# Kernel tuning notes

Hardware: AMD Instinct MI355X
Metric: run time of the kernel (lower is better)

Reference implementation:

```python
import jax, jax.numpy as jnp
import numpy as np

M_FEATS = 1536      # number of proposals (docstring: [M, K])
K_DIM = 128         # feature dim per docstring example
NUM_CLASSES = 16    # label vocabulary; torch.unique loop becomes a fixed class sweep


def setup_inputs() -> dict:
    key = jax.random.key(0)
    k1, k2 = jax.random.split(key)
    features = jax.random.normal(k1, (M_FEATS, K_DIM), dtype=jnp.float32)
    labels = jax.random.randint(k2, (M_FEATS,), 0, NUM_CLASSES, dtype=jnp.int32)
    # ious all ones -> keep = (ious >= 0.5) is all-True, so the boolean filter is identity
    ious = jnp.ones((M_FEATS,), dtype=jnp.float32)
    return {"features": features, "labels": labels, "ious": ious}


def reference(features, labels, ious):
    # reweight_func='none' -> coef = ones_like(ious); keep mask is all-True by construction
    coef = jnp.ones_like(ious)
    # similarity [M, M]; coef broadcasts over columns, matching `similarity * coef` in torch
    sim = jnp.matmul(features, features.T) * coef[None, :]
    m = sim.shape[0]
    eye = jnp.eye(m, dtype=sim.dtype)
    # ground set term: logdet(similarity + 0.5 I)  (mask_ground is all ones)
    ground = jnp.linalg.slogdet(sim + 0.5 * eye)[1]

    # Per-label logdet of the submatrix S_c + 0.5 I_{n_c}. Instead of extracting a
    # variable-size submatrix (not jit-able), embed it in a full [M, M] matrix that is
    # block-diagonal: class block = S_c + 0.5 I, off-class diagonal = 1. Its logdet
    # equals logdet(S_c + 0.5 I). Absent classes give identity -> logdet 0, matching
    # torch.unique skipping them.
    onehot = (labels[:, None] == jnp.arange(NUM_CLASSES, dtype=labels.dtype)[None, :])
    onehot = onehot.astype(sim.dtype)  # [M, C]

    def class_logdet(mask):  # mask: [M] 0/1 indicator for one class
        A = sim * (mask[:, None] * mask[None, :]) + jnp.diag(0.5 * mask + (1.0 - mask))
        return jnp.linalg.slogdet(A)[1]

    per_class = jax.vmap(class_logdet)(onehot.T)  # [C]
    loss = jnp.sum(per_class) - ground
    return loss  # scalar; .mean() of a scalar is itself
```

## Files before the change

kernel.cpp:

```cpp
#include <hip/hip_runtime.h>
#include <math.h>


#define M_FEATS 1536
#define K_DIM 128
#define NUM_CLASSES 16
#define GRAM_ELEMS (K_DIM * K_DIM)
#define PIDX(i) ((i) + ((i) >> 4))
#define SENT 0x13579BDF
#define MP 104
#define ALD 132

typedef short bf16x8 __attribute__((ext_vector_type(8)));
typedef float f32x4 __attribute__((ext_vector_type(4)));

__device__ __forceinline__ short f2bf(float x) {
    unsigned u = __float_as_uint(x);
    u += 0x7FFFu + ((u >> 16) & 1u);
    return (short)(u >> 16);
}

__device__ __forceinline__ float chol128(
    float A[8][8], const int t, const int rg, const int cg,
    const int i0, const int j0,
    float4* panLo, float4* panHi, float4* wshLo, float4* wshHi, float* logp)
{
    if (rg == 0) {
#pragma unroll
        for (int q = 0; q < 8; ++q) {
            panLo[PIDX(j0 + q)] = make_float4(A[0][q], A[1][q], A[2][q], A[3][q]);
            panHi[PIDX(j0 + q)] = make_float4(A[4][q], A[5][q], A[6][q], A[7][q]);
        }
    }

#pragma unroll 1
    for (int s = 0; s < 16; ++s) {
        const int k = 8 * s;
        __syncthreads();

        if (t < K_DIM) {
            float4 dL[8], dH[8];
#pragma unroll
            for (int c = 0; c < 8; ++c) {
                dL[c] = panLo[PIDX(k + c)];
                dH[c] = panHi[PIDX(k + c)];
            }
            float4 aL = panLo[PIDX(t)], aH = panHi[PIDX(t)];

            float D[8][8];
#pragma unroll
            for (int c = 0; c < 8; ++c) {
                D[0][c] = dL[c].x; D[1][c] = dL[c].y;
                D[2][c] = dL[c].z; D[3][c] = dL[c].w;
                D[4][c] = dH[c].x; D[5][c] = dH[c].y;
                D[6][c] = dH[c].z; D[7][c] = dH[c].w;
            }

            float L[8][8], ic[8];
            float prod = 1.0f;
#pragma unroll
            for (int c = 0; c < 8; ++c) {
                float v = D[c][c];
#pragma unroll
                for (int m = 0; m < c; ++m) v = fmaf(-L[c][m], L[c][m], v);
                prod *= v;
                ic[c] = rsqrtf(v);
#pragma unroll
                for (int r = c + 1; r < 8; ++r) {
                    float x = D[r][c];
#pragma unroll
                    for (int m = 0; m < c; ++m) x = fmaf(-L[r][m], L[c][m], x);
                    L[r][c] = x * ic[c];
                }
            }
            if (t == 0) logp[s] = prod;

            float a[8] = {aL.x, aL.y, aL.z, aL.w, aH.x, aH.y, aH.z, aH.w};
            float w[8];
#pragma unroll
            for (int c = 0; c < 8; ++c) {
                float x = a[c];
#pragma unroll
                for (int m = 0; m < c; ++m) x = fmaf(-L[c][m], w[m], x);
                w[c] = x * ic[c];
            }
            wshLo[PIDX(t)] = make_float4(w[0], w[1], w[2], w[3]);
            wshHi[PIDX(t)] = make_float4(w[4], w[5], w[6], w[7]);
        }
        __syncthreads();

        if (rg > s && cg > s) {
            float4 wrL[8], wrH[8];
#pragma unroll
            for (int r = 0; r < 8; ++r) {
                wrL[r] = wshLo[PIDX(i0 + r)];
                wrH[r] = wshHi[PIDX(i0 + r)];
            }
#pragma unroll
            for (int q = 0; q < 8; ++q) {
                float4 wjL = wshLo[PIDX(j0 + q)];
                float4 wjH = wshHi[PIDX(j0 + q)];
#pragma unroll
                for (int r = 0; r < 8; ++r) {
                    float x = A[r][q];
                    x = fmaf(-wrL[r].x, wjL.x, x);
                    x = fmaf(-wrL[r].y, wjL.y, x);
                    x = fmaf(-wrL[r].z, wjL.z, x);
                    x = fmaf(-wrL[r].w, wjL.w, x);
                    x = fmaf(-wrH[r].x, wjH.x, x);
                    x = fmaf(-wrH[r].y, wjH.y, x);
                    x = fmaf(-wrH[r].z, wjH.z, x);
                    x = fmaf(-wrH[r].w, wjH.w, x);
                    A[r][q] = x;
                }
            }
        }
        if (rg == s + 1) {
#pragma unroll
            for (int q = 0; q < 8; ++q) {
                panLo[PIDX(j0 + q)] = make_float4(A[0][q], A[1][q], A[2][q], A[3][q]);
                panHi[PIDX(j0 + q)] = make_float4(A[4][q], A[5][q], A[6][q], A[7][q]);
            }
        }
    }

    float ls = 0.0f;
    if (t == 0) {
#pragma unroll
        for (int s = 0; s < 16; ++s) ls += logf(logp[s]);
    }
    return ls;
}

__global__ __launch_bounds__(256, 1) void fused_kernel(
    const float* __restrict__ f, const int* __restrict__ labels,
    float* __restrict__ groundG, float* __restrict__ ldet,
    int* __restrict__ flagG, int* __restrict__ flag3,
    float* __restrict__ out)
{
    __shared__ int cnt;
    __shared__ int list[M_FEATS];
    __shared__ short FT[K_DIM * MP];
    __shared__ float Agram[K_DIM * ALD];
    __shared__ float4 panLo[136], panHi[136], wshLo[136], wshHi[136];
    __shared__ float logp[16];

    const int b = blockIdx.x;
    const int t = threadIdx.x;
    const int rg = t >> 4;
    const int cg = t & 15;
    const int i0 = rg << 3;
    const int j0 = cg << 3;

    float A[8][8];

    if (b < NUM_CLASSES) {
        const int cls = b;
        if (t == 0) cnt = 0;
        __syncthreads();
        {
            const int lane = t & 63;
            const unsigned long long ltmask = (lane == 63)
                ? 0x7FFFFFFFFFFFFFFFull : ((1ull << lane) - 1ull);
#pragma unroll
            for (int it = 0; it < M_FEATS / 256; ++it) {
                const int i = it * 256 + t;
                const bool pred = (labels[i] == cls);
                const unsigned long long mask = __ballot(pred);
                int base = 0;
                if (lane == 0 && mask)
                    base = atomicAdd(&cnt, __popcll(mask));
                base = __shfl(base, 0);
                if (pred)
                    list[base + __popcll(mask & ltmask)] = i;
            }
        }
        __syncthreads();
        const int n = cnt;

        const int wave = t >> 6, lane = t & 63, ln = lane & 15, quad = lane >> 4;
        const int mlane = t & 31, cgrp = t >> 5;

        f32x4 acc[2][8];
#pragma unroll
        for (int x = 0; x < 2; ++x)
#pragma unroll
            for (int tc = 0; tc < 8; ++tc)
                acc[x][tc] = (f32x4){0.f, 0.f, 0.f, 0.f};

        const int nchunks = (n + 95) / 96;
        for (int ch = 0; ch < nchunks; ++ch) {
            const int cb = ch * 96;
#pragma unroll
            for (int it = 0; it < 12; ++it) {
                const int m = (it % 3) * 32 + mlane;
                const int cgp = (it / 3) * 8 + cgrp;
                const int gm = cb + m;
                float4 v = make_float4(0.f, 0.f, 0.f, 0.f);
                if (gm < n) {
                    const int src = list[gm];
                    v = *(const float4*)(f + (size_t)src * K_DIM + cgp * 4);
                }
                FT[(cgp * 4 + 0) * MP + m] = f2bf(v.x);
                FT[(cgp * 4 + 1) * MP + m] = f2bf(v.y);
                FT[(cgp * 4 + 2) * MP + m] = f2bf(v.z);
                FT[(cgp * 4 + 3) * MP + m] = f2bf(v.w);
            }
            __syncthreads();
#pragma unroll
            for (int kc = 0; kc < 3; ++kc) {
                const int kb = kc * 32 + quad * 8;
                bf16x8 a0 = *(const bf16x8*)(FT + ((wave * 2 + 0) * 16 + ln) * MP + kb);
                bf16x8 a1 = *(const bf16x8*)(FT + ((wave * 2 + 1) * 16 + ln) * MP + kb);
#pragma unroll
                for (int tc = 0; tc < 8; ++tc) {
                    bf16x8 bb = *(const bf16x8*)(FT + (tc * 16 + ln) * MP + kb);
                    acc[0][tc] = __builtin_amdgcn_mfma_f32_16x16x32_bf16(
                        a0, bb, acc[0][tc], 0, 0, 0);
                    acc[1][tc] = __builtin_amdgcn_mfma_f32_16x16x32_bf16(
                        a1, bb, acc[1][tc], 0, 0, 0);
                }
            }
            __syncthreads();
        }

#pragma unroll
        for (int x = 0; x < 2; ++x)
#pragma unroll
            for (int tc = 0; tc < 8; ++tc)
#pragma unroll
                for (int rr = 0; rr < 4; ++rr) {
                    const int row = (wave * 2 + x) * 16 + quad * 4 + rr;
                    const int col = tc * 16 + ln;
                    const float v = acc[x][tc][rr];
                    Agram[row * ALD + col] = v;
                    unsafeAtomicAdd(&groundG[row * K_DIM + col], v);
                }
        __syncthreads();
        if (t == 0)
            __hip_atomic_store(&flagG[cls], SENT, __ATOMIC_RELEASE,
                               __HIP_MEMORY_SCOPE_AGENT);

#pragma unroll
        for (int r = 0; r < 8; ++r) {
            float4 v0 = *(const float4*)(Agram + (i0 + r) * ALD + j0);
            float4 v1 = *(const float4*)(Agram + (i0 + r) * ALD + j0 + 4);
            A[r][0] = v0.x; A[r][1] = v0.y; A[r][2] = v0.z; A[r][3] = v0.w;
            A[r][4] = v1.x; A[r][5] = v1.y; A[r][6] = v1.z; A[r][7] = v1.w;
        }
#pragma unroll
        for (int r = 0; r < 8; ++r)
#pragma unroll
            for (int q = 0; q < 8; ++q)
                if ((i0 + r) == (j0 + q)) A[r][q] += 0.5f;

        float ls = chol128(A, t, rg, cg, i0, j0, panLo, panHi, wshLo, wshHi, logp);

        if (t == 0) {
            ldet[cls] = ls;
            __hip_atomic_store(&flag3[cls], SENT, __ATOMIC_RELEASE,
                               __HIP_MEMORY_SCOPE_AGENT);
        }
        return;
    }

    if (t < NUM_CLASSES)
        while (__hip_atomic_load(&flagG[t], __ATOMIC_ACQUIRE,
                                 __HIP_MEMORY_SCOPE_AGENT) != SENT)
            __builtin_amdgcn_s_sleep(2);
    __syncthreads();

#pragma unroll
    for (int r = 0; r < 8; ++r) {
        float4 v0 = *(const float4*)(groundG + (i0 + r) * K_DIM + j0);
        float4 v1 = *(const float4*)(groundG + (i0 + r) * K_DIM + j0 + 4);
        A[r][0] = v0.x; A[r][1] = v0.y; A[r][2] = v0.z; A[r][3] = v0.w;
        A[r][4] = v1.x; A[r][5] = v1.y; A[r][6] = v1.z; A[r][7] = v1.w;
    }
#pragma unroll
    for (int r = 0; r < 8; ++r)
#pragma unroll
        for (int q = 0; q < 8; ++q)
            if ((i0 + r) == (j0 + q)) A[r][q] += 0.5f;

    float ls = chol128(A, t, rg, cg, i0, j0, panLo, panHi, wshLo, wshHi, logp);

    if (t < NUM_CLASSES)
        while (__hip_atomic_load(&flag3[t], __ATOMIC_ACQUIRE,
                                 __HIP_MEMORY_SCOPE_AGENT) != SENT)
            __builtin_amdgcn_s_sleep(2);
    __syncthreads();

    if (t == 0) {
        float total = 1920.0f * 0.6931471805599453f - ls;
#pragma unroll
        for (int c = 0; c < NUM_CLASSES; ++c) total += ldet[c];
        out[0] = total;
    }
}

extern "C" void kernel_launch(void* const* d_in, const int* in_sizes, int n_in,
                              void* d_out, int out_size, void* d_ws, size_t ws_size,
                              hipStream_t stream)
{
    const float* features = (const float*)d_in[0];
    const int* labels = (const int*)d_in[1];

    float* groundG = (float*)d_ws;
    float* ldetp   = groundG + GRAM_ELEMS;
    int* flagG     = (int*)(ldetp + NUM_CLASSES);
    int* flag3     = flagG + NUM_CLASSES;

    fused_kernel<<<NUM_CLASSES + 1, 256, 0, stream>>>(
        features, labels, groundG, ldetp, flagG, flag3, (float*)d_out);
}
```

Before: 97.67 us.

## Overlap next panel factorization with trailing update and use packed FMA

Restructures the blocked Cholesky loop so that the 8-column panel factor/solve for step s+1 runs right after the panel-owning row group finishes its update. The remaining trailing-update columns of the other threads are applied after that, which shortens the critical path per step. The trailing update is also rewritten to use 2-wide vector FMAs (packed fp32) on pre-transposed w pairs. This adds register pressure (wjp, wrL/wrH kept live across the barrier) and changes the per-thread workload split.

```diff
diff --git a/kernel.cpp b/kernel.cpp
--- a/kernel.cpp
+++ b/kernel.cpp
@@ -13,6 +13,7 @@
 
 typedef short bf16x8 __attribute__((ext_vector_type(8)));
 typedef float f32x4 __attribute__((ext_vector_type(4)));
+typedef float f32x2 __attribute__((ext_vector_type(2)));
 
 __device__ __forceinline__ short f2bf(float x) {
     unsigned u = __float_as_uint(x);
@@ -20,6 +21,92 @@
     return (short)(u >> 16);
 }
 
+__device__ __forceinline__ void chol_chain(
+    const int ss, const int t,
+    const float4* panLo, const float4* panHi,
+    float4* wshLo, float4* wshHi, float* logp)
+{
+    const int k = 8 * ss;
+    float4 dL[8], dH[8];
+#pragma unroll
+    for (int c = 0; c < 8; ++c) {
+        dL[c] = panLo[PIDX(k + c)];
+        dH[c] = panHi[PIDX(k + c)];
+    }
+    float4 aL = panLo[PIDX(t)], aH = panHi[PIDX(t)];
+
+    float D[8][8];
+#pragma unroll
+    for (int c = 0; c < 8; ++c) {
+        D[0][c] = dL[c].x; D[1][c] = dL[c].y;
+        D[2][c] = dL[c].z; D[3][c] = dL[c].w;
+        D[4][c] = dH[c].x; D[5][c] = dH[c].y;
+        D[6][c] = dH[c].z; D[7][c] = dH[c].w;
+    }
+
+    float L[8][8], ic[8];
+    float prod = 1.0f;
+#pragma unroll
+    for (int c = 0; c < 8; ++c) {
+        float v = D[c][c];
+#pragma unroll
+        for (int m = 0; m < c; ++m) v = fmaf(-L[c][m], L[c][m], v);
+        prod *= v;
+        ic[c] = rsqrtf(v);
+#pragma unroll
+        for (int r = c + 1; r < 8; ++r) {
+            float x = D[r][c];
+#pragma unroll
+            for (int m = 0; m < c; ++m) x = fmaf(-L[r][m], L[c][m], x);
+            L[r][c] = x * ic[c];
+        }
+    }
+    if (t == 0) logp[ss] = prod;
+
+    float a[8] = {aL.x, aL.y, aL.z, aL.w, aH.x, aH.y, aH.z, aH.w};
+    float w[8];
+#pragma unroll
+    for (int c = 0; c < 8; ++c) {
+        float x = a[c];
+#pragma unroll
+        for (int m = 0; m < c; ++m) x = fmaf(-L[c][m], w[m], x);
+        w[c] = x * ic[c];
+    }
+    wshLo[PIDX(t)] = make_float4(w[0], w[1], w[2], w[3]);
+    wshHi[PIDX(t)] = make_float4(w[4], w[5], w[6], w[7]);
+}
+
+template <int Q2LO, int Q2HI>
+__device__ __forceinline__ void trail_update(
+    float A[8][8], const float4* wrL, const float4* wrH, const f32x2 (*wjp)[4])
+{
+#pragma unroll
+    for (int r = 0; r < 8; ++r) {
+        const f32x2 n0 = (f32x2){-wrL[r].x, -wrL[r].x};
+        const f32x2 n1 = (f32x2){-wrL[r].y, -wrL[r].y};
+        const f32x2 n2 = (f32x2){-wrL[r].z, -wrL[r].z};
+        const f32x2 n3 = (f32x2){-wrL[r].w, -wrL[r].w};
+        const f32x2 n4 = (f32x2){-wrH[r].x, -wrH[r].x};
+        const f32x2 n5 = (f32x2){-wrH[r].y, -wrH[r].y};
+        const f32x2 n6 = (f32x2){-wrH[r].z, -wrH[r].z};
+        const f32x2 n7 = (f32x2){-wrH[r].w, -wrH[r].w};
+#pragma unroll
+        for (int q2 = Q2LO; q2 < Q2HI; ++q2) {
+            f32x2 x = (f32x2){A[r][2 * q2], A[r][2 * q2 + 1]};
+            x = __builtin_elementwise_fma(n0, wjp[0][q2], x);
+            x = __builtin_elementwise_fma(n1, wjp[1][q2], x);
+            x = __builtin_elementwise_fma(n2, wjp[2][q2], x);
+            x = __builtin_elementwise_fma(n3, wjp[3][q2], x);
+            x = __builtin_elementwise_fma(n4, wjp[4][q2], x);
+            x = __builtin_elementwise_fma(n5, wjp[5][q2], x);
+            x = __builtin_elementwise_fma(n6, wjp[6][q2], x);
+            x = __builtin_elementwise_fma(n7, wjp[7][q2], x);
+            A[r][2 * q2]     = x.x;
+            A[r][2 * q2 + 1] = x.y;
+        }
+    }
+}
+
 __device__ __forceinline__ float chol128(
     float A[8][8], const int t, const int rg, const int cg,
     const int i0, const int j0,
@@ -32,65 +119,17 @@
             panHi[PIDX(j0 + q)] = make_float4(A[4][q], A[5][q], A[6][q], A[7][q]);
         }
     }
+    __syncthreads();
+    if (t < K_DIM) chol_chain(0, t, panLo, panHi, wshLo, wshHi, logp);
 
 #pragma unroll 1
-    for (int s = 0; s < 16; ++s) {
-        const int k = 8 * s;
-        __syncthreads();
-
-        if (t < K_DIM) {
-            float4 dL[8], dH[8];
-#pragma unroll
-            for (int c = 0; c < 8; ++c) {
-                dL[c] = panLo[PIDX(k + c)];
-                dH[c] = panHi[PIDX(k + c)];
-            }
-            float4 aL = panLo[PIDX(t)], aH = panHi[PIDX(t)];
-
-            float D[8][8];
-#pragma unroll
-            for (int c = 0; c < 8; ++c) {
-                D[0][c] = dL[c].x; D[1][c] = dL[c].y;
-                D[2][c] = dL[c].z; D[3][c] = dL[c].w;
-                D[4][c] = dH[c].x; D[5][c] = dH[c].y;
-                D[6][c] = dH[c].z; D[7][c] = dH[c].w;
-            }
-
-            float L[8][8], ic[8];
-            float prod = 1.0f;
-#pragma unroll
-            for (int c = 0; c < 8; ++c) {
-                float v = D[c][c];
-#pragma unroll
-                for (int m = 0; m < c; ++m) v = fmaf(-L[c][m], L[c][m], v);
-                prod *= v;
-                ic[c] = rsqrtf(v);
-#pragma unroll
-                for (int r = c + 1; r < 8; ++r) {
-                    float x = D[r][c];
-#pragma unroll
-                    for (int m = 0; m < c; ++m) x = fmaf(-L[r][m], L[c][m], x);
-                    L[r][c] = x * ic[c];
-                }
-            }
-            if (t == 0) logp[s] = prod;
-
-            float a[8] = {aL.x, aL.y, aL.z, aL.w, aH.x, aH.y, aH.z, aH.w};
-            float w[8];
-#pragma unroll
-            for (int c = 0; c < 8; ++c) {
-                float x = a[c];
-#pragma unroll
-                for (int m = 0; m < c; ++m) x = fmaf(-L[c][m], w[m], x);
-                w[c] = x * ic[c];
-            }
-            wshLo[PIDX(t)] = make_float4(w[0], w[1], w[2], w[3]);
-            wshHi[PIDX(t)] = make_float4(w[4], w[5], w[6], w[7]);
-        }
-        __syncthreads();
-
-        if (rg > s && cg > s) {
-            float4 wrL[8], wrH[8];
+    for (int s = 0; s < 15; ++s) {
+        __syncthreads();
+        const bool act = (rg > s) && (cg > s);
+        float4 wrL[8], wrH[8];
+        f32x2 wjp[8][4];
+        if (act) {
+            float4 wjL[8], wjH[8];
 #pragma unroll
             for (int r = 0; r < 8; ++r) {
                 wrL[r] = wshLo[PIDX(i0 + r)];
@@ -98,22 +137,24 @@
             }
 #pragma unroll
             for (int q = 0; q < 8; ++q) {
-                float4 wjL = wshLo[PIDX(j0 + q)];
-                float4 wjH = wshHi[PIDX(j0 + q)];
-#pragma unroll
-                for (int r = 0; r < 8; ++r) {
-                    float x = A[r][q];
-                    x = fmaf(-wrL[r].x, wjL.x, x);
-                    x = fmaf(-wrL[r].y, wjL.y, x);
-                    x = fmaf(-wrL[r].z, wjL.z, x);
-                    x = fmaf(-wrL[r].w, wjL.w, x);
-                    x = fmaf(-wrH[r].x, wjH.x, x);
-                    x = fmaf(-wrH[r].y, wjH.y, x);
-                    x = fmaf(-wrH[r].z, wjH.z, x);
-                    x = fmaf(-wrH[r].w, wjH.w, x);
-                    A[r][q] = x;
-                }
-            }
+                wjL[q] = wshLo[PIDX(j0 + q)];
+                wjH[q] = wshHi[PIDX(j0 + q)];
+            }
+#pragma unroll
+            for (int q2 = 0; q2 < 4; ++q2) {
+                const float4 pa = wjL[2 * q2], pb = wjL[2 * q2 + 1];
+                const float4 pc = wjH[2 * q2], pd = wjH[2 * q2 + 1];
+                wjp[0][q2] = (f32x2){pa.x, pb.x};
+                wjp[1][q2] = (f32x2){pa.y, pb.y};
+                wjp[2][q2] = (f32x2){pa.z, pb.z};
+                wjp[3][q2] = (f32x2){pa.w, pb.w};
+                wjp[4][q2] = (f32x2){pc.x, pd.x};
+                wjp[5][q2] = (f32x2){pc.y, pd.y};
+                wjp[6][q2] = (f32x2){pc.z, pd.z};
+                wjp[7][q2] = (f32x2){pc.w, pd.w};
+            }
+            if (rg == s + 1) trail_update<0, 4>(A, wrL, wrH, wjp);
+            else             trail_update<0, 2>(A, wrL, wrH, wjp);
         }
         if (rg == s + 1) {
 #pragma unroll
@@ -122,12 +163,15 @@
                 panHi[PIDX(j0 + q)] = make_float4(A[4][q], A[5][q], A[6][q], A[7][q]);
             }
         }
+        __syncthreads();
+        if (t < K_DIM) chol_chain(s + 1, t, panLo, panHi, wshLo, wshHi, logp);
+        if (act && rg != s + 1) trail_update<2, 4>(A, wrL, wrH, wjp);
     }
 
     float ls = 0.0f;
     if (t == 0) {
 #pragma unroll
-        for (int s = 0; s < 16; ++s) ls += logf(logp[s]);
+        for (int ss = 0; ss < 16; ++ss) ls += logf(logp[ss]);
     }
     return ls;
 }
```

After: 109.0 us. 1.12x slower.

## Move Cholesky trailing update onto MFMA with bf16 hi/lo split accumulation

Applied to the files above, without the earlier changes.

Replaces the per-thread FP32 register trailing update in the blocked 128x128 Cholesky with MFMA bf16 matrix ops. The panel vector is split into high and low bf16 parts so that precision stays close to FP32. Updates accumulate into a running MFMA accumulator of W·Wᵀ, and each step rebuilds its 8-row strip as the original Gram block minus that accumulator. The aim is to cut the VALU FMA cost of the serial 16-step factorization. The trade-off is extra shared memory staging, some precision risk from the bf16 split, and redundant MFMA work on already-factored tiles.

```diff
diff --git a/kernel.cpp b/kernel.cpp
--- a/kernel.cpp
+++ b/kernel.cpp
@@ -6,10 +6,10 @@
 #define K_DIM 128
 #define NUM_CLASSES 16
 #define GRAM_ELEMS (K_DIM * K_DIM)
-#define PIDX(i) ((i) + ((i) >> 4))
 #define SENT 0x13579BDF
 #define MP 104
 #define ALD 132
+#define WS 24
 
 typedef short bf16x8 __attribute__((ext_vector_type(8)));
 typedef float f32x4 __attribute__((ext_vector_type(4)));
@@ -20,41 +20,57 @@
     return (short)(u >> 16);
 }
 
-__device__ __forceinline__ float chol128(
-    float A[8][8], const int t, const int rg, const int cg,
-    const int i0, const int j0,
-    float4* panLo, float4* panHi, float4* wshLo, float4* wshHi, float* logp)
+__device__ __forceinline__ float chol128_mfma(
+    const int t, const float* __restrict__ Agram, float* __restrict__ strip,
+    short* __restrict__ Whl, float* __restrict__ logp)
 {
-    if (rg == 0) {
-#pragma unroll
-        for (int q = 0; q < 8; ++q) {
-            panLo[PIDX(j0 + q)] = make_float4(A[0][q], A[1][q], A[2][q], A[3][q]);
-            panHi[PIDX(j0 + q)] = make_float4(A[4][q], A[5][q], A[6][q], A[7][q]);
-        }
-    }
+    const int wave = t >> 6, lane = t & 63, ln = lane & 15, quad = lane >> 4;
+
+    f32x4 acc[2][8];
+#pragma unroll
+    for (int x = 0; x < 2; ++x)
+#pragma unroll
+        for (int tc = 0; tc < 8; ++tc)
+            acc[x][tc] = (f32x4){0.f, 0.f, 0.f, 0.f};
 
 #pragma unroll 1
     for (int s = 0; s < 16; ++s) {
         const int k = 8 * s;
+
+        const int sb = s >> 1, sw = sb >> 1, sx = sb & 1, sq = (s & 1) * 2;
+        if (wave == sw && (quad == sq || quad == sq + 1)) {
+            const int qrel = quad - sq;
+            const int rbase = (sw * 2 + sx) * 16 + quad * 4;
+            if (sx == 0) {
+#pragma unroll
+                for (int tc = 0; tc < 8; ++tc)
+#pragma unroll
+                    for (int rr = 0; rr < 4; ++rr)
+                        strip[(qrel * 4 + rr) * 128 + tc * 16 + ln] =
+                            Agram[(rbase + rr) * ALD + tc * 16 + ln] - acc[0][tc][rr];
+            } else {
+#pragma unroll
+                for (int tc = 0; tc < 8; ++tc)
+#pragma unroll
+                    for (int rr = 0; rr < 4; ++rr)
+                        strip[(qrel * 4 + rr) * 128 + tc * 16 + ln] =
+                            Agram[(rbase + rr) * ALD + tc * 16 + ln] - acc[1][tc][rr];
+            }
+        }
         __syncthreads();
 
         if (t < K_DIM) {
-            float4 dL[8], dH[8];
-#pragma unroll
-            for (int c = 0; c < 8; ++c) {
-                dL[c] = panLo[PIDX(k + c)];
-                dH[c] = panHi[PIDX(k + c)];
-            }
-            float4 aL = panLo[PIDX(t)], aH = panHi[PIDX(t)];
-
             float D[8][8];
 #pragma unroll
-            for (int c = 0; c < 8; ++c) {
-                D[0][c] = dL[c].x; D[1][c] = dL[c].y;
-                D[2][c] = dL[c].z; D[3][c] = dL[c].w;
-                D[4][c] = dH[c].x; D[5][c] = dH[c].y;
-                D[6][c] = dH[c].z; D[7][c] = dH[c].w;
-            }
+            for (int r = 0; r < 8; ++r) {
+                float4 d0 = *(const float4*)(strip + r * 128 + k);
+                float4 d1 = *(const float4*)(strip + r * 128 + k + 4);
+                D[r][0] = d0.x; D[r][1] = d0.y; D[r][2] = d0.z; D[r][3] = d0.w;
+                D[r][4] = d1.x; D[r][5] = d1.y; D[r][6] = d1.z; D[r][7] = d1.w;
+            }
+            float a[8];
+#pragma unroll
+            for (int c = 0; c < 8; ++c) a[c] = strip[c * 128 + t];
 
             float L[8][8], ic[8];
             float prod = 1.0f;
@@ -75,7 +91,6 @@
             }
             if (t == 0) logp[s] = prod;
 
-            float a[8] = {aL.x, aL.y, aL.z, aL.w, aH.x, aH.y, aH.z, aH.w};
             float w[8];
 #pragma unroll
             for (int c = 0; c < 8; ++c) {
@@ -84,42 +99,62 @@
                 for (int m = 0; m < c; ++m) x = fmaf(-L[c][m], w[m], x);
                 w[c] = x * ic[c];
             }
-            wshLo[PIDX(t)] = make_float4(w[0], w[1], w[2], w[3]);
-            wshHi[PIDX(t)] = make_float4(w[4], w[5], w[6], w[7]);
-        }
-        __syncthreads();
-
-        if (rg > s && cg > s) {
-            float4 wrL[8], wrH[8];
-#pragma unroll
-            for (int r = 0; r < 8; ++r) {
-                wrL[r] = wshLo[PIDX(i0 + r)];
-                wrH[r] = wshHi[PIDX(i0 + r)];
-            }
-#pragma unroll
-            for (int q = 0; q < 8; ++q) {
-                float4 wjL = wshLo[PIDX(j0 + q)];
-                float4 wjH = wshHi[PIDX(j0 + q)];
-#pragma unroll
-                for (int r = 0; r < 8; ++r) {
-                    float x = A[r][q];
-                    x = fmaf(-wrL[r].x, wjL.x, x);
-                    x = fmaf(-wrL[r].y, wjL.y, x);
-                    x = fmaf(-wrL[r].z, wjL.z, x);
-                    x = fmaf(-wrL[r].w, wjL.w, x);
-                    x = fmaf(-wrH[r].x, wjH.x, x);
-                    x = fmaf(-wrH[r].y, wjH.y, x);
-                    x = fmaf(-wrH[r].z, wjH.z, x);
-                    x = fmaf(-wrH[r].w, wjH.w, x);
-                    A[r][q] = x;
-                }
-            }
-        }
-        if (rg == s + 1) {
-#pragma unroll
-            for (int q = 0; q < 8; ++q) {
-                panLo[PIDX(j0 + q)] = make_float4(A[0][q], A[1][q], A[2][q], A[3][q]);
-                panHi[PIDX(j0 + q)] = make_float4(A[4][q], A[5][q], A[6][q], A[7][q]);
+            if (t < k) {
+#pragma unroll
+                for (int c = 0; c < 8; ++c) w[c] = 0.f;
+            }
+
+            unsigned uh[4], ul[4];
+#pragma unroll
+            for (int j = 0; j < 4; ++j) {
+                const float w0 = w[2 * j], w1 = w[2 * j + 1];
+                const unsigned h0 = (unsigned short)f2bf(w0);
+                const unsigned h1 = (unsigned short)f2bf(w1);
+                const float f0 = __uint_as_float(h0 << 16);
+                const float f1 = __uint_as_float(h1 << 16);
+                const unsigned l0 = (unsigned short)f2bf(w0 - f0);
+                const unsigned l1 = (unsigned short)f2bf(w1 - f1);
+                uh[j] = (h1 << 16) | h0;
+                ul[j] = (l1 << 16) | l0;
+            }
+            *(int4*)(Whl + t * WS) =
+                make_int4((int)uh[0], (int)uh[1], (int)uh[2], (int)uh[3]);
+            *(int4*)(Whl + t * WS + 8) =
+                make_int4((int)ul[0], (int)ul[1], (int)ul[2], (int)ul[3]);
+        }
+        __syncthreads();
+
+        const int live = 8 * (s + 1);
+        const bool live0 = ((wave * 2 + 0) * 16 + 16) > live;
+        const bool live1 = ((wave * 2 + 1) * 16 + 16) > live;
+        if (live0 | live1) {
+            const bf16x8 z = {};
+            const short* a0p = Whl + (((wave * 2 + 0) * 16 + ln) * WS) + (quad & 1) * 8;
+            const short* a1p = Whl + (((wave * 2 + 1) * 16 + ln) * WS) + (quad & 1) * 8;
+            bf16x8 a0 = *(const bf16x8*)a0p;
+            bf16x8 a1 = *(const bf16x8*)a1p;
+            a0 = (quad < 2) ? a0 : z;
+            a1 = (quad < 2) ? a1 : z;
+#pragma unroll
+            for (int tc = 0; tc < 8; ++tc) {
+                if ((tc * 16 + 16) <= live) continue;
+                const short* bp = Whl + (tc * 16 + ln) * WS;
+                bf16x8 bh = *(const bf16x8*)(bp);
+                bf16x8 bl = *(const bf16x8*)(bp + 8);
+                bh = (quad < 2) ? bh : z;
+                bl = (quad < 2) ? bl : z;
+                if (live0) {
+                    acc[0][tc] = __builtin_amdgcn_mfma_f32_16x16x32_bf16(
+                        a0, bh, acc[0][tc], 0, 0, 0);
+                    acc[0][tc] = __builtin_amdgcn_mfma_f32_16x16x32_bf16(
+                        a0, bl, acc[0][tc], 0, 0, 0);
+                }
+                if (live1) {
+                    acc[1][tc] = __builtin_amdgcn_mfma_f32_16x16x32_bf16(
+                        a1, bh, acc[1][tc], 0, 0, 0);
+                    acc[1][tc] = __builtin_amdgcn_mfma_f32_16x16x32_bf16(
+                        a1, bl, acc[1][tc], 0, 0, 0);
+                }
             }
         }
     }
@@ -127,7 +162,7 @@
     float ls = 0.0f;
     if (t == 0) {
 #pragma unroll
-        for (int s = 0; s < 16; ++s) ls += logf(logp[s]);
+        for (int ss = 0; ss < 16; ++ss) ls += logf(logp[ss]);
     }
     return ls;
 }
@@ -140,19 +175,14 @@
 {
     __shared__ int cnt;
     __shared__ int list[M_FEATS];
-    __shared__ short FT[K_DIM * MP];
-    __shared__ float Agram[K_DIM * ALD];
-    __shared__ float4 panLo[136], panHi[136], wshLo[136], wshHi[136];
+    __shared__ __align__(16) short FT[K_DIM * MP];
+    __shared__ __align__(16) float Agram[K_DIM * ALD];
+    __shared__ __align__(16) float strip[8 * 128];
+    __shared__ __align__(16) short Whl[K_DIM * WS];
     __shared__ float logp[16];
 
     const int b = blockIdx.x;
     const int t = threadIdx.x;
-    const int rg = t >> 4;
-    const int cg = t & 15;
-    const int i0 = rg << 3;
-    const int j0 = cg << 3;
-
-    float A[8][8];
 
     if (b < NUM_CLASSES) {
         const int cls = b;
@@ -241,20 +271,10 @@
             __hip_atomic_store(&flagG[cls], SENT, __ATOMIC_RELEASE,
                                __HIP_MEMORY_SCOPE_AGENT);
 
-#pragma unroll
-        for (int r = 0; r < 8; ++r) {
-            float4 v0 = *(const float4*)(Agram + (i0 + r) * ALD + j0);
-            float4 v1 = *(const float4*)(Agram + (i0 + r) * ALD + j0 + 4);
-            A[r][0] = v0.x; A[r][1] = v0.y; A[r][2] = v0.z; A[r][3] = v0.w;
-            A[r][4] = v1.x; A[r][5] = v1.y; A[r][6] = v1.z; A[r][7] = v1.w;
-        }
-#pragma unroll
-        for (int r = 0; r < 8; ++r)
-#pragma unroll
-            for (int q = 0; q < 8; ++q)
-                if ((i0 + r) == (j0 + q)) A[r][q] += 0.5f;
-
-        float ls = chol128(A, t, rg, cg, i0, j0, panLo, panHi, wshLo, wshHi, logp);
+        if (t < K_DIM) Agram[t * ALD + t] += 0.5f;
+        __syncthreads();
+
+        float ls = chol128_mfma(t, Agram, strip, Whl, logp);
 
         if (t == 0) {
             ldet[cls] = ls;
@@ -271,19 +291,17 @@
     __syncthreads();
 
 #pragma unroll
-    for (int r = 0; r < 8; ++r) {
-        float4 v0 = *(const float4*)(groundG + (i0 + r) * K_DIM + j0);
-        float4 v1 = *(const float4*)(groundG + (i0 + r) * K_DIM + j0 + 4);
-        A[r][0] = v0.x; A[r][1] = v0.y; A[r][2] = v0.z; A[r][3] = v0.w;
-        A[r][4] = v1.x; A[r][5] = v1.y; A[r][6] = v1.z; A[r][7] = v1.w;
-    }
-#pragma unroll
-    for (int r = 0; r < 8; ++r)
-#pragma unroll
-        for (int q = 0; q < 8; ++q)
-            if ((i0 + r) == (j0 + q)) A[r][q] += 0.5f;
-
-    float ls = chol128(A, t, rg, cg, i0, j0, panLo, panHi, wshLo, wshHi, logp);
+    for (int j = 0; j < 16; ++j) {
+        const int idx = j * 256 + t;
+        const int row = idx >> 5, c4 = idx & 31;
+        *(float4*)(Agram + row * ALD + c4 * 4) =
+            *(const float4*)(groundG + (size_t)idx * 4);
+    }
+    __syncthreads();
+    if (t < K_DIM) Agram[t * ALD + t] += 0.5f;
+    __syncthreads();
+
+    float ls = chol128_mfma(t, Agram, strip, Whl, logp);
 
     if (t < NUM_CLASSES)
         while (__hip_atomic_load(&flag3[t], __ATOMIC_ACQUIRE,
```

After: 100.6 us. 3.0% more time.
